# Performance work log

Hardware: AMD Instinct MI355X
Metric: run time of the kernel (lower is better)

The kernel has to match this reference:

```python
import jax, jax.numpy as jnp
import numpy as np
import math

EPS = 1e-15
R_CUT = 5.0
BERN_K = 16
FEAT = 128
N_ATOMS = 16384
N_EDGES = 100000
# log binomial(BERN_K-1, k) for the Bernstein radial basis
LOG_BINOM = np.array([math.lgamma(BERN_K) - math.lgamma(k + 1) - math.lgamma(BERN_K - k)
                      for k in range(BERN_K)], dtype=np.float32)


def swish(x, a, b):
    # learnable swish: a * x * sigmoid(b * x)
    return a * x * jax.nn.sigmoid(b * x)


def resmlp(x, W1, b1, W2, b2, Wout, aa, bb):
    # Residual( PreAct(lin1) -> PreAct(lin2) ) -> act -> Linear(no bias)
    h = swish(x, aa[0], bb[0]) @ W1.T + b1
    h = swish(h, aa[1], bb[1]) @ W2.T + b2
    y = x + h
    return swish(y, aa[2], bb[2]) @ Wout.T


def sph_harm(u, l):
    ux, uy, uz = u[:, 0], u[:, 1], u[:, 2]
    if l == 0:
        return jnp.ones((u.shape[0], 1), u.dtype)
    if l == 1:
        return jnp.stack([uy, uz, ux], axis=-1)
    s3 = 3.0 ** 0.5
    return jnp.stack([s3 * ux * uy, s3 * uy * uz, 0.5 * (3.0 * uz ** 2 - 1.0),
                      s3 * ux * uz, 0.5 * s3 * (ux ** 2 - uy ** 2)], axis=-1)


def bernstein_rho(r, gamma):
    # rho_k(r) = C(K-1,k) x^k (1-x)^(K-1-k) * f_cut(r), x = exp(-gamma r)
    k = jnp.arange(BERN_K, dtype=r.dtype)
    x = jnp.exp(-gamma * r)[:, None]                      # (E,1)
    bern = jnp.exp(jnp.asarray(LOG_BINOM)) * x ** k * (1.0 - x) ** (BERN_K - 1 - k)
    inside = r < R_CUT
    denom = jnp.where(inside, R_CUT ** 2 - r ** 2, 1.0)
    fcut = jnp.where(inside, jnp.exp(-r ** 2 / denom), 0.0)
    return bern * fcut[:, None]                           # (E,K)


def setup_inputs() -> dict:
    key = jax.random.key(0)
    ks = jax.random.split(key, 16)
    D, K = FEAT, BERN_K
    sc = 1.0 / (D ** 0.5)
    inp = {
        'xyz': jax.random.normal(ks[0], (N_ATOMS, 3), jnp.float32),
        'x_tilde': jax.random.normal(ks[1], (N_ATOMS, D), jnp.float32),
        'nbrs': jax.random.randint(ks[2], (N_EDGES, 2), 0, N_ATOMS),
        # 5 ResidualMLPs stacked: order [c, s, p, d, l]
        'W1': jax.random.normal(ks[3], (5, D, D), jnp.float32) * sc,
        'b1': jnp.zeros((5, D), jnp.float32),
        'W2': jax.random.normal(ks[4], (5, D, D), jnp.float32) * sc,
        'b2': jnp.zeros((5, D), jnp.float32),
        'Wout': jax.random.normal(ks[5], (5, D, D), jnp.float32) * sc,
        'act_a': jnp.ones((5, 3), jnp.float32),
        'act_b': jnp.full((5, 3), 1.702, jnp.float32),
        'G_s': jax.random.normal(ks[6], (D, K), jnp.float32) * (1.0 / K ** 0.5),
        'G_p': jax.random.normal(ks[7], (D, K), jnp.float32) * (1.0 / K ** 0.5),
        'G_d': jax.random.normal(ks[8], (D, K), jnp.float32) * (1.0 / K ** 0.5),
        'P_1': jax.random.normal(ks[9], (D, D), jnp.float32) * sc,
        'P_2': jax.random.normal(ks[10], (D, D), jnp.float32) * sc,
        'D_1': jax.random.normal(ks[11], (D, D), jnp.float32) * sc,
        'D_2': jax.random.normal(ks[12], (D, D), jnp.float32) * sc,
        'gamma': jnp.asarray(0.5, jnp.float32),
    }
    return inp


def reference(xyz, x_tilde, nbrs, W1, b1, W2, b2, Wout, act_a, act_b,
              G_s, G_p, G_d, P_1, P_2, D_1, D_2, gamma):
    N = xyz.shape[0]
    src = nbrs[:, 0]
    dst = nbrs[:, 1]
    r_ij = xyz[dst] - xyz[src]                            # (E,3)
    r = jnp.sqrt((r_ij ** 2 + EPS).sum(-1))               # stable norm, (E,)
    u = r_ij / r[:, None]
    rho = bernstein_rho(r, gamma)                         # (E,K)
    x_j = x_tilde[dst]                                    # (E,D)

    def mlp(x, i):
        return resmlp(x, W1[i], b1[i], W2[i], b2[i], Wout[i], act_a[i], act_b[i])

    c_term = mlp(x_tilde, 0)                              # (N,D)

    quants = []
    for i, (l, G) in enumerate([(0, G_s), (1, G_p), (2, G_d)]):
        y = sph_harm(u, l)                                # (E,M)
        # fused g_matmul: G @ (rho (x) y) -> (E,D,M), avoids (E,K,M) temp
        gm = jnp.einsum('dk,ek,em->edm', G, rho, y)
        feat = mlp(x_j, i + 1)                            # (E,D)
        per_nbr = feat[:, :, None] * gm                   # (E,D,M)
        quants.append(jax.ops.segment_sum(per_nbr, src, num_segments=N))

    def take_inner(q, M1, M2):
        t1 = jnp.einsum('ij,njm->nim', M1, q)
        t2 = jnp.einsum('ij,njm->nim', M2, q)
        return (t1 * t2).sum(-1)                          # (N,D)

    inp = c_term + quants[0][:, :, 0] \
        + take_inner(quants[1], P_1, P_2) + take_inner(quants[2], D_1, D_2)
    return mlp(inp, 4)
```

## Files before the change

kernel.cpp:

```cpp
#include <hip/hip_runtime.h>
#include <math.h>

#define D 128

typedef __attribute__((ext_vector_type(8))) short short8v;
typedef __attribute__((ext_vector_type(4))) float f32x4;
typedef __attribute__((ext_vector_type(4))) unsigned int uint4v;

__device__ __forceinline__ float fast_swish(float v, float a, float b) {
  float e = __builtin_amdgcn_exp2f(-1.4426950408889634f * (b * v));
  return a * v * __builtin_amdgcn_rcpf(1.0f + e);
}

__device__ __forceinline__ void bf16split_rne(float v, unsigned short& h, unsigned short& l) {
  unsigned int u = __float_as_uint(v);
  unsigned int rh = (u + 0x7FFFu + ((u >> 16) & 1u)) & 0xFFFF0000u;
  h = (unsigned short)(rh >> 16);
  float lf = v - __uint_as_float(rh);
  unsigned int u2 = __float_as_uint(lf);
  unsigned int rl = u2 + 0x7FFFu + ((u2 >> 16) & 1u);
  l = (unsigned short)(rl >> 16);
}

__device__ __forceinline__ void bf16split_fast(float v, unsigned short& h, unsigned short& l) {
  unsigned int u = __float_as_uint(v);
  h = (unsigned short)(u >> 16);
  float lf = v - __uint_as_float(u & 0xFFFF0000u);
  unsigned int u2 = __float_as_uint(lf);
  l = (unsigned short)((u2 + 0x7FFFu + ((u2 >> 16) & 1u)) >> 16);
}

template <bool SW>
__device__ __forceinline__ void stage16(const float* __restrict__ src, int lane,
                                        unsigned short* shHi, unsigned short* shLo,
                                        float a, float b) {
#pragma unroll
  for (int i = 0; i < 4; ++i) {
    int t = lane + 64 * i;
    int r = t >> 4, c = t & 15;
    const float4 v0 = *(const float4*)(src + r * D + c * 8);
    const float4 v1 = *(const float4*)(src + r * D + c * 8 + 4);
    float vv[8] = {v0.x, v0.y, v0.z, v0.w, v1.x, v1.y, v1.z, v1.w};
    unsigned int hw[4], lw[4];
#pragma unroll
    for (int jj = 0; jj < 4; ++jj) {
      float x0 = SW ? fast_swish(vv[2 * jj], a, b) : vv[2 * jj];
      float x1 = SW ? fast_swish(vv[2 * jj + 1], a, b) : vv[2 * jj + 1];
      unsigned short h0, l0, h1, l1;
      bf16split_fast(x0, h0, l0);
      bf16split_fast(x1, h1, l1);
      hw[jj] = (unsigned int)h0 | ((unsigned int)h1 << 16);
      lw[jj] = (unsigned int)l0 | ((unsigned int)l1 << 16);
    }
    int off = (c * 16) ^ ((r & 7) << 4);
    uint4v hv = {hw[0], hw[1], hw[2], hw[3]};
    uint4v lv = {lw[0], lw[1], lw[2], lw[3]};
    *(uint4v*)((char*)(shHi + r * D) + off) = hv;
    *(uint4v*)((char*)(shLo + r * D) + off) = lv;
  }
}

__device__ __forceinline__ void load_afrags(const unsigned short* sh, int lane, short8v* f) {
  int rl = lane & 15, q = lane >> 4;
  const char* base = (const char*)(sh + rl * D);
#pragma unroll
  for (int kc = 0; kc < 4; ++kc) {
    int off = (kc * 64 + q * 16) ^ ((rl & 7) << 4);
    f[kc] = *(const short8v*)(base + off);
  }
}

__device__ __forceinline__ void gemm16(const short8v* ah, const short8v* al,
                                       const unsigned short* __restrict__ prep, int m,
                                       int lane, f32x4* accs) {
  const short8v* ph = (const short8v*)(prep + (size_t)(2 * m) * 16384);
  const short8v* pl = (const short8v*)(prep + (size_t)(2 * m + 1) * 16384);
#pragma unroll
  for (int nt = 0; nt < 8; ++nt) {
    f32x4 acc = {0.f, 0.f, 0.f, 0.f};
#pragma unroll
    for (int kc = 0; kc < 4; ++kc) {
      int ci = (nt * 4 + kc) * 64 + lane;
      short8v bh = ph[ci];
      short8v bl = pl[ci];
      acc = __builtin_amdgcn_mfma_f32_16x16x32_bf16(al[kc], bh, acc, 0, 0, 0);
      acc = __builtin_amdgcn_mfma_f32_16x16x32_bf16(ah[kc], bl, acc, 0, 0, 0);
      acc = __builtin_amdgcn_mfma_f32_16x16x32_bf16(ah[kc], bh, acc, 0, 0, 0);
    }
    accs[nt] = acc;
  }
}

__global__ void prep_weights_kernel(const float* __restrict__ W1, const float* __restrict__ W2,
                                    const float* __restrict__ Wo, const float* __restrict__ P1,
                                    const float* __restrict__ P2, const float* __restrict__ D1,
                                    const float* __restrict__ D2, unsigned short* __restrict__ prep) {
  int t = blockIdx.x * 256 + threadIdx.x;
  if (t >= 19 * 2048) return;
  int m = t >> 11;
  int rem = t & 2047;
  int nt = rem >> 8;
  int kc = (rem >> 6) & 3;
  int lane = rem & 63;
  const float* src;
  if (m < 5) src = W1 + (size_t)m * 16384;
  else if (m < 10) src = W2 + (size_t)(m - 5) * 16384;
  else if (m < 15) src = Wo + (size_t)(m - 10) * 16384;
  else if (m == 15) src = P1;
  else if (m == 16) src = P2;
  else if (m == 17) src = D1;
  else src = D2;
  int row = nt * 16 + (lane & 15);
  int k0 = kc * 32 + (lane >> 4) * 8;
  unsigned int hw[4], lw[4];
#pragma unroll
  for (int jj = 0; jj < 4; ++jj) {
    unsigned short h0, l0, h1, l1;
    bf16split_rne(src[row * D + k0 + 2 * jj], h0, l0);
    bf16split_rne(src[row * D + k0 + 2 * jj + 1], h1, l1);
    hw[jj] = (unsigned int)h0 | ((unsigned int)h1 << 16);
    lw[jj] = (unsigned int)l0 | ((unsigned int)l1 << 16);
  }
  size_t chunk = (size_t)((nt * 4 + kc) * 64 + lane);
  uint4v hv = {hw[0], hw[1], hw[2], hw[3]};
  uint4v lv = {lw[0], lw[1], lw[2], lw[3]};
  *(uint4v*)(prep + (size_t)(2 * m) * 16384 + chunk * 8) = hv;
  *(uint4v*)(prep + (size_t)(2 * m + 1) * 16384 + chunk * 8) = lv;
}

__global__ __launch_bounds__(256) void resmlp_mfma(
    const float* __restrict__ xin, const unsigned short* __restrict__ prep,
    const float* __restrict__ b1b, const float* __restrict__ b2b,
    const float* __restrict__ act_a, const float* __restrict__ act_b,
    float* __restrict__ outbase, int branch_off, int n_atoms)
{
  __shared__ __align__(16) unsigned short shHiA[4][16 * D];
  __shared__ __align__(16) unsigned short shLoA[4][16 * D];
  const int lane = threadIdx.x & 63;
  const int wid = threadIdx.x >> 6;
  unsigned short* shHi = shHiA[wid];
  unsigned short* shLo = shLoA[wid];
  const int atom0 = (blockIdx.x * 4 + wid) * 16;
  const int br = blockIdx.y + branch_off;
  const float* b1 = b1b + br * D;
  const float* b2 = b2b + br * D;
  const float a0 = act_a[br * 3 + 0], g0 = act_b[br * 3 + 0];
  const float a1 = act_a[br * 3 + 1], g1 = act_b[br * 3 + 1];
  const float a2 = act_a[br * 3 + 2], g2 = act_b[br * 3 + 2];
  float* out = outbase + (size_t)blockIdx.y * n_atoms * D;
  const float* x0 = xin + (size_t)atom0 * D;

  stage16<true>(x0, lane, shHi, shLo, a0, g0);

  const int rl = lane & 15;
  const int rowq = (lane >> 4) * 4;
  short8v ah[4], al[4];
  f32x4 accs[8];

  load_afrags(shHi, lane, ah);
  load_afrags(shLo, lane, al);
  gemm16(ah, al, prep, br, lane, accs);
#pragma unroll
  for (int nt = 0; nt < 8; ++nt) {
    int col = nt * 16 + rl;
    float bv = b1[col];
#pragma unroll
    for (int r = 0; r < 4; ++r) {
      int row = rowq + r;
      float s = fast_swish(accs[nt][r] + bv, a1, g1);
      unsigned short h, l;
      bf16split_fast(s, h, l);
      int off = (col * 2) ^ ((row & 7) << 4);
      *(unsigned short*)((char*)(shHi + row * D) + off) = h;
      *(unsigned short*)((char*)(shLo + row * D) + off) = l;
    }
  }

  load_afrags(shHi, lane, ah);
  load_afrags(shLo, lane, al);
  gemm16(ah, al, prep, 5 + br, lane, accs);
#pragma unroll
  for (int nt = 0; nt < 8; ++nt) {
    int col = nt * 16 + rl;
    float bv = b2[col];
#pragma unroll
    for (int r = 0; r < 4; ++r) {
      int row = rowq + r;
      float y = x0[row * D + col] + accs[nt][r] + bv;
      float s = fast_swish(y, a2, g2);
      unsigned short h, l;
      bf16split_fast(s, h, l);
      int off = (col * 2) ^ ((row & 7) << 4);
      *(unsigned short*)((char*)(shHi + row * D) + off) = h;
      *(unsigned short*)((char*)(shLo + row * D) + off) = l;
    }
  }

  load_afrags(shHi, lane, ah);
  load_afrags(shLo, lane, al);
  gemm16(ah, al, prep, 10 + br, lane, accs);
#pragma unroll
  for (int nt = 0; nt < 8; ++nt)
#pragma unroll
    for (int r = 0; r < 4; ++r)
      out[(size_t)(atom0 + rowq + r) * D + nt * 16 + rl] = accs[nt][r];
}

__global__ __launch_bounds__(256) void inner_mfma(
    const float* __restrict__ q1, const float* __restrict__ q2,
    const unsigned short* __restrict__ prep,
    float* __restrict__ pA, float* __restrict__ pB, int n_atoms)
{
  __shared__ __align__(16) unsigned short shHiA[4][16 * D];
  __shared__ __align__(16) unsigned short shLoA[4][16 * D];
  const int lane = threadIdx.x & 63;
  const int wid = threadIdx.x >> 6;
  unsigned short* shHi = shHiA[wid];
  unsigned short* shLo = shLoA[wid];
  const int atom0 = (blockIdx.x * 4 + wid) * 16;
  const int g = blockIdx.y;
  const size_t nd = (size_t)n_atoms * D;
  const int rl = lane & 15;
  const int rowq = (lane >> 4) * 4;
  f32x4 eacc[8];
#pragma unroll
  for (int nt = 0; nt < 8; ++nt) eacc[nt] = f32x4{0.f, 0.f, 0.f, 0.f};

  for (int pp = 0; pp < 2; ++pp) {
    const int part = g * 2 + pp;
    const float* qp = (part < 3) ? q1 + (size_t)part * nd : q2 + (size_t)(part - 3) * nd;
    const int m1 = (part < 3) ? 15 : 17;
    stage16<false>(qp + (size_t)atom0 * D, lane, shHi, shLo, 0.f, 0.f);
    short8v ah[4], al[4];
    load_afrags(shHi, lane, ah);
    load_afrags(shLo, lane, al);
    const short8v* p1h = (const short8v*)(prep + (size_t)(2 * m1) * 16384);
    const short8v* p1l = (const short8v*)(prep + (size_t)(2 * m1 + 1) * 16384);
    const short8v* p2h = (const short8v*)(prep + (size_t)(2 * m1 + 2) * 16384);
    const short8v* p2l = (const short8v*)(prep + (size_t)(2 * m1 + 3) * 16384);
#pragma unroll
    for (int nt = 0; nt < 8; ++nt) {
      f32x4 t1 = {0.f, 0.f, 0.f, 0.f}, t2 = {0.f, 0.f, 0.f, 0.f};
#pragma unroll
      for (int kc = 0; kc < 4; ++kc) {
        int ci = (nt * 4 + kc) * 64 + lane;
        short8v b1h = p1h[ci], b1l = p1l[ci];
        short8v b2h = p2h[ci], b2l = p2l[ci];
        t1 = __builtin_amdgcn_mfma_f32_16x16x32_bf16(al[kc], b1h, t1, 0, 0, 0);
        t1 = __builtin_amdgcn_mfma_f32_16x16x32_bf16(ah[kc], b1l, t1, 0, 0, 0);
        t1 = __builtin_amdgcn_mfma_f32_16x16x32_bf16(ah[kc], b1h, t1, 0, 0, 0);
        t2 = __builtin_amdgcn_mfma_f32_16x16x32_bf16(al[kc], b2h, t2, 0, 0, 0);
        t2 = __builtin_amdgcn_mfma_f32_16x16x32_bf16(ah[kc], b2l, t2, 0, 0, 0);
        t2 = __builtin_amdgcn_mfma_f32_16x16x32_bf16(ah[kc], b2h, t2, 0, 0, 0);
      }
      eacc[nt] += t1 * t2;
    }
  }
  float* outp = (g < 3) ? (pA + (size_t)g * nd) : pB;
#pragma unroll
  for (int nt = 0; nt < 8; ++nt)
#pragma unroll
    for (int r = 0; r < 4; ++r)
      outp[(size_t)(atom0 + rowq + r) * D + nt * 16 + rl] = eacc[nt][r];
}

__global__ void edge_geom_kernel(const float* __restrict__ xyz,
                                 const int* __restrict__ nbrs,
                                 const float* __restrict__ gamma_p,
                                 float* __restrict__ rho_ws,
                                 float* __restrict__ y_ws, int n_edges)
{
  int e = blockIdx.x * 256 + threadIdx.x;
  if (e >= n_edges) return;
  int s = nbrs[2 * e], dd = nbrs[2 * e + 1];
  float rx = xyz[3 * dd + 0] - xyz[3 * s + 0];
  float ry = xyz[3 * dd + 1] - xyz[3 * s + 1];
  float rz = xyz[3 * dd + 2] - xyz[3 * s + 2];
  float r2 = rx * rx + ry * ry + rz * rz + 3e-15f;
  float r = sqrtf(r2);
  float inv = 1.0f / r;
  float ux = rx * inv, uy = ry * inv, uz = rz * inv;
  float gamma = gamma_p[0];
  float xv = __expf(-gamma * r);
  float omx = 1.0f - xv;
  float fcut = 0.0f;
  if (r < 5.0f) fcut = __expf(-r2 / (25.0f - r2));
  float xp[16], op[16];
  xp[0] = 1.f; op[0] = 1.f;
#pragma unroll
  for (int k = 1; k < 16; ++k) { xp[k] = xp[k - 1] * xv; op[k] = op[k - 1] * omx; }
  const float C[16] = {1.f, 15.f, 105.f, 455.f, 1365.f, 3003.f, 5005.f, 6435.f,
                       6435.f, 5005.f, 3003.f, 1365.f, 455.f, 105.f, 15.f, 1.f};
  float* rp = rho_ws + (size_t)e * 16;
#pragma unroll
  for (int k = 0; k < 16; ++k) rp[k] = C[k] * xp[k] * op[15 - k] * fcut;
  const float s3 = 1.7320508075688772f;
  float* yp = y_ws + (size_t)e * 8;
  yp[0] = uy; yp[1] = uz; yp[2] = ux;
  yp[3] = s3 * ux * uy; yp[4] = s3 * uy * uz; yp[5] = 0.5f * (3.f * uz * uz - 1.f);
  yp[6] = s3 * ux * uz; yp[7] = 0.5f * s3 * (ux * ux - uy * uy);
}

__global__ void hist_kernel(const int* __restrict__ nbrs, int* __restrict__ counts, int n_edges) {
  int e = blockIdx.x * 256 + threadIdx.x;
  if (e < n_edges) atomicAdd(&counts[nbrs[2 * e]], 1);
}

__global__ __launch_bounds__(1024) void scan_kernel(const int* __restrict__ counts,
                                                    int* __restrict__ offsets, int n) {
  __shared__ int part[1024];
  int tid = threadIdx.x;
  int base = tid * 16;
  int loc[16]; int s = 0;
#pragma unroll
  for (int i = 0; i < 16; ++i) {
    int c = (base + i < n) ? counts[base + i] : 0;
    loc[i] = c; s += c;
  }
  part[tid] = s;
  __syncthreads();
  for (int off = 1; off < 1024; off <<= 1) {
    int v = (tid >= off) ? part[tid - off] : 0;
    __syncthreads();
    part[tid] += v;
    __syncthreads();
  }
  int run = (tid == 0) ? 0 : part[tid - 1];
#pragma unroll
  for (int i = 0; i < 16; ++i) {
    if (base + i < n) offsets[base + i] = run;
    run += loc[i];
  }
}

__global__ void scatter_kernel(const int* __restrict__ nbrs, const int* __restrict__ offsets,
                               int* __restrict__ cursor, int* __restrict__ sorted, int n_edges) {
  int e = blockIdx.x * 256 + threadIdx.x;
  if (e < n_edges) {
    int s = nbrs[2 * e];
    int pos = offsets[s] + atomicAdd(&cursor[s], 1);
    sorted[pos] = e;
  }
}

__global__ __launch_bounds__(128) void aggregate_kernel(
    const float* __restrict__ rho_ws, const float* __restrict__ y_ws,
    const int* __restrict__ nbrs, const int* __restrict__ offsets,
    const int* __restrict__ counts, const int* __restrict__ sorted,
    const float* __restrict__ feat1, const float* __restrict__ feat2,
    const float* __restrict__ feat3,
    const float* __restrict__ Gs, const float* __restrict__ Gp,
    const float* __restrict__ Gd,
    float* __restrict__ q0, float* __restrict__ q1, float* __restrict__ q2,
    int n_atoms)
{
  int n = blockIdx.x;
  int d = threadIdx.x;
  float gs[16], gp[16], gd[16];
#pragma unroll
  for (int c = 0; c < 4; ++c) {
    float4 v = *(const float4*)&Gs[d * 16 + 4 * c];
    gs[4 * c] = v.x; gs[4 * c + 1] = v.y; gs[4 * c + 2] = v.z; gs[4 * c + 3] = v.w;
    v = *(const float4*)&Gp[d * 16 + 4 * c];
    gp[4 * c] = v.x; gp[4 * c + 1] = v.y; gp[4 * c + 2] = v.z; gp[4 * c + 3] = v.w;
    v = *(const float4*)&Gd[d * 16 + 4 * c];
    gd[4 * c] = v.x; gd[4 * c + 1] = v.y; gd[4 * c + 2] = v.z; gd[4 * c + 3] = v.w;
  }
  float a0 = 0.f, a1[3] = {0.f, 0.f, 0.f}, a2[5] = {0.f, 0.f, 0.f, 0.f, 0.f};
  int off = offsets[n], cnt = counts[n];
  for (int i = 0; i < cnt; ++i) {
    int e = sorted[off + i];
    int dst = nbrs[2 * e + 1];
    const float4* rp = (const float4*)(rho_ws + (size_t)e * 16);
    float4 r0v = rp[0], r1v = rp[1], r2v = rp[2], r3v = rp[3];
    float rho[16] = {r0v.x, r0v.y, r0v.z, r0v.w, r1v.x, r1v.y, r1v.z, r1v.w,
                     r2v.x, r2v.y, r2v.z, r2v.w, r3v.x, r3v.y, r3v.z, r3v.w};
    const float4* ypv = (const float4*)(y_ws + (size_t)e * 8);
    float4 y0v = ypv[0], y1v = ypv[1];
    float g_s = 0.f, g_p = 0.f, g_d = 0.f;
#pragma unroll
    for (int k = 0; k < 16; ++k) {
      g_s += gs[k] * rho[k];
      g_p += gp[k] * rho[k];
      g_d += gd[k] * rho[k];
    }
    float f1 = feat1[(size_t)dst * D + d];
    float f2 = feat2[(size_t)dst * D + d];
    float f3 = feat3[(size_t)dst * D + d];
    a0 += f1 * g_s;
    float ap = f2 * g_p;
    a1[0] += ap * y0v.x; a1[1] += ap * y0v.y; a1[2] += ap * y0v.z;
    float ad = f3 * g_d;
    a2[0] += ad * y0v.w; a2[1] += ad * y1v.x; a2[2] += ad * y1v.y;
    a2[3] += ad * y1v.z; a2[4] += ad * y1v.w;
  }
  q0[(size_t)n * D + d] = a0;
#pragma unroll
  for (int m = 0; m < 3; ++m) q1[((size_t)m * n_atoms + n) * D + d] = a1[m];
#pragma unroll
  for (int m = 0; m < 5; ++m) q2[((size_t)m * n_atoms + n) * D + d] = a2[m];
}

__global__ void assemble_kernel(const float* __restrict__ cterm,
                                const float* __restrict__ q0,
                                const float* __restrict__ pA,
                                const float* __restrict__ pB,
                                float* __restrict__ inp, int nd4)
{
  int i = blockIdx.x * 256 + threadIdx.x;
  if (i >= nd4) return;
  const float4* c = (const float4*)cterm;
  const float4* z = (const float4*)q0;
  const float4* a = (const float4*)pA;
  const float4* b = (const float4*)pB;
  float4 v = c[i], zz = z[i];
  float4 a0 = a[i], a1 = a[i + (size_t)nd4], a2 = a[i + 2 * (size_t)nd4], bb = b[i];
  float4 r;
  r.x = v.x + zz.x + a0.x + a1.x + a2.x + bb.x;
  r.y = v.y + zz.y + a0.y + a1.y + a2.y + bb.y;
  r.z = v.z + zz.z + a0.z + a1.z + a2.z + bb.z;
  r.w = v.w + zz.w + a0.w + a1.w + a2.w + bb.w;
  ((float4*)inp)[i] = r;
}

extern "C" void kernel_launch(void* const* d_in, const int* in_sizes, int n_in,
                              void* d_out, int out_size, void* d_ws, size_t ws_size,
                              hipStream_t stream)
{
  const float* xyz     = (const float*)d_in[0];
  const float* x_tilde = (const float*)d_in[1];
  const int*   nbrs    = (const int*)d_in[2];
  const float* W1      = (const float*)d_in[3];
  const float* b1      = (const float*)d_in[4];
  const float* W2      = (const float*)d_in[5];
  const float* b2      = (const float*)d_in[6];
  const float* Wout    = (const float*)d_in[7];
  const float* act_a   = (const float*)d_in[8];
  const float* act_b   = (const float*)d_in[9];
  const float* Gs      = (const float*)d_in[10];
  const float* Gp      = (const float*)d_in[11];
  const float* Gd      = (const float*)d_in[12];
  const float* P1      = (const float*)d_in[13];
  const float* P2      = (const float*)d_in[14];
  const float* D1m     = (const float*)d_in[15];
  const float* D2m     = (const float*)d_in[16];
  const float* gamma   = (const float*)d_in[17];
  float* out = (float*)d_out;

  const int n_atoms = in_sizes[0] / 3;
  const int n_edges = in_sizes[2] / 2;

  float* ws = (float*)d_ws;
  size_t nd = (size_t)n_atoms * D;
  float* feats  = ws;
  float* q0     = feats + 4 * nd;
  float* q1     = q0 + nd;
  float* q2     = q1 + 3 * nd;
  float* rho_ws = q2 + 5 * nd;
  float* y_ws   = rho_ws + (size_t)n_edges * 16;
  float* inp    = y_ws + (size_t)n_edges * 8;
  int* counts  = (int*)(inp + nd);
  int* offsets = counts + n_atoms;
  int* cursor  = offsets + n_atoms;
  int* sorted  = cursor + n_atoms;
  unsigned short* prep =
      (unsigned short*)(((uintptr_t)(sorted + n_edges) + 15) & ~(uintptr_t)15);

  float* pA = feats + nd;
  float* pB = rho_ws;

  hipMemsetAsync(counts, 0, (size_t)n_atoms * sizeof(int), stream);
  hipMemsetAsync(cursor, 0, (size_t)n_atoms * sizeof(int), stream);

  dim3 blk(256);
  int eb = (n_edges + 255) / 256;

  prep_weights_kernel<<<(19 * 2048 + 255) / 256, blk, 0, stream>>>(
      W1, W2, Wout, P1, P2, D1m, D2m, prep);

  resmlp_mfma<<<dim3(n_atoms / 64, 4), dim3(256), 0, stream>>>(
      x_tilde, prep, b1, b2, act_a, act_b, feats, 0, n_atoms);

  edge_geom_kernel<<<eb, blk, 0, stream>>>(xyz, nbrs, gamma, rho_ws, y_ws, n_edges);
  hist_kernel<<<eb, blk, 0, stream>>>(nbrs, counts, n_edges);
  scan_kernel<<<1, 1024, 0, stream>>>(counts, offsets, n_atoms);
  scatter_kernel<<<eb, blk, 0, stream>>>(nbrs, offsets, cursor, sorted, n_edges);

  aggregate_kernel<<<n_atoms, 128, 0, stream>>>(
      rho_ws, y_ws, nbrs, offsets, counts, sorted,
      feats + nd, feats + 2 * nd, feats + 3 * nd, Gs, Gp, Gd,
      q0, q1, q2, n_atoms);

  inner_mfma<<<dim3(n_atoms / 64, 4), dim3(256), 0, stream>>>(
      q1, q2, prep, pA, pB, n_atoms);

  assemble_kernel<<<(int)((nd / 4 + 255) / 256), blk, 0, stream>>>(
      feats, q0, pA, pB, inp, (int)(nd / 4));

  resmlp_mfma<<<dim3(n_atoms / 64, 1), dim3(256), 0, stream>>>(
      inp, prep, b1, b2, act_a, act_b, out, 4, n_atoms);
}
```

Measured before the change: 340.3 us.

## Share 64-row activation tile across warps, split output columns per warp

The resmlp and inner MFMA kernels now stage a shared 64-row activation tile per block instead of a private 16-row tile per warp. Each warp computes two 16-column output tiles across all 64 rows rather than all 128 columns for 16 rows. Each warp therefore loads only a quarter of the weight fragments from global or L2 and reuses each across four row tiles. The cost is block-wide __syncthreads between layers, and A fragments are now re-read from LDS for every k-chunk instead of being held in registers.

```diff
diff --git a/kernel.cpp b/kernel.cpp
--- a/kernel.cpp
+++ b/kernel.cpp
@@ -28,6 +28,13 @@
   float lf = v - __uint_as_float(u & 0xFFFF0000u);
   unsigned int u2 = __float_as_uint(lf);
   l = (unsigned short)((u2 + 0x7FFFu + ((u2 >> 16) & 1u)) >> 16);
+}
+
+__device__ __forceinline__ f32x4 mfma3(short8v ah, short8v al, short8v bh, short8v bl, f32x4 acc) {
+  acc = __builtin_amdgcn_mfma_f32_16x16x32_bf16(al, bh, acc, 0, 0, 0);
+  acc = __builtin_amdgcn_mfma_f32_16x16x32_bf16(ah, bl, acc, 0, 0, 0);
+  acc = __builtin_amdgcn_mfma_f32_16x16x32_bf16(ah, bh, acc, 0, 0, 0);
+  return acc;
 }
 
 template <bool SW>
@@ -57,37 +64,6 @@
     uint4v lv = {lw[0], lw[1], lw[2], lw[3]};
     *(uint4v*)((char*)(shHi + r * D) + off) = hv;
     *(uint4v*)((char*)(shLo + r * D) + off) = lv;
-  }
-}
-
-__device__ __forceinline__ void load_afrags(const unsigned short* sh, int lane, short8v* f) {
-  int rl = lane & 15, q = lane >> 4;
-  const char* base = (const char*)(sh + rl * D);
-#pragma unroll
-  for (int kc = 0; kc < 4; ++kc) {
-    int off = (kc * 64 + q * 16) ^ ((rl & 7) << 4);
-    f[kc] = *(const short8v*)(base + off);
-  }
-}
-
-__device__ __forceinline__ void gemm16(const short8v* ah, const short8v* al,
-                                       const unsigned short* __restrict__ prep, int m,
-                                       int lane, f32x4* accs) {
-  const short8v* ph = (const short8v*)(prep + (size_t)(2 * m) * 16384);
-  const short8v* pl = (const short8v*)(prep + (size_t)(2 * m + 1) * 16384);
-#pragma unroll
-  for (int nt = 0; nt < 8; ++nt) {
-    f32x4 acc = {0.f, 0.f, 0.f, 0.f};
-#pragma unroll
-    for (int kc = 0; kc < 4; ++kc) {
-      int ci = (nt * 4 + kc) * 64 + lane;
-      short8v bh = ph[ci];
-      short8v bl = pl[ci];
-      acc = __builtin_amdgcn_mfma_f32_16x16x32_bf16(al[kc], bh, acc, 0, 0, 0);
-      acc = __builtin_amdgcn_mfma_f32_16x16x32_bf16(ah[kc], bl, acc, 0, 0, 0);
-      acc = __builtin_amdgcn_mfma_f32_16x16x32_bf16(ah[kc], bh, acc, 0, 0, 0);
-    }
-    accs[nt] = acc;
   }
 }
 
@@ -134,13 +110,11 @@
     const float* __restrict__ act_a, const float* __restrict__ act_b,
     float* __restrict__ outbase, int branch_off, int n_atoms)
 {
-  __shared__ __align__(16) unsigned short shHiA[4][16 * D];
-  __shared__ __align__(16) unsigned short shLoA[4][16 * D];
+  __shared__ __align__(16) unsigned short shHi[64 * D];
+  __shared__ __align__(16) unsigned short shLo[64 * D];
   const int lane = threadIdx.x & 63;
   const int wid = threadIdx.x >> 6;
-  unsigned short* shHi = shHiA[wid];
-  unsigned short* shLo = shLoA[wid];
-  const int atom0 = (blockIdx.x * 4 + wid) * 16;
+  const int atom0 = blockIdx.x * 64;
   const int br = blockIdx.y + branch_off;
   const float* b1 = b1b + br * D;
   const float* b2 = b2b + br * D;
@@ -150,60 +124,92 @@
   float* out = outbase + (size_t)blockIdx.y * n_atoms * D;
   const float* x0 = xin + (size_t)atom0 * D;
 
-  stage16<true>(x0, lane, shHi, shLo, a0, g0);
+  stage16<true>(x0 + wid * 16 * D, lane, shHi + wid * 16 * D, shLo + wid * 16 * D, a0, g0);
+  __syncthreads();
 
   const int rl = lane & 15;
-  const int rowq = (lane >> 4) * 4;
-  short8v ah[4], al[4];
-  f32x4 accs[8];
-
-  load_afrags(shHi, lane, ah);
-  load_afrags(shLo, lane, al);
-  gemm16(ah, al, prep, br, lane, accs);
-#pragma unroll
-  for (int nt = 0; nt < 8; ++nt) {
-    int col = nt * 16 + rl;
+  const int q = lane >> 4;
+  const int rowq = q * 4;
+  const int nt0 = wid * 2;
+
+  f32x4 acc[4][2];
+
+#define GEMM_LAYER(mat)                                                        \
+  do {                                                                         \
+    const unsigned short* ph = prep + (size_t)(2 * (mat)) * 16384;             \
+    const unsigned short* pl = prep + (size_t)(2 * (mat) + 1) * 16384;         \
+    _Pragma("unroll") for (int mt = 0; mt < 4; ++mt)                           \
+        _Pragma("unroll") for (int j = 0; j < 2; ++j)                          \
+            acc[mt][j] = f32x4{0.f, 0.f, 0.f, 0.f};                            \
+    _Pragma("unroll") for (int kc = 0; kc < 4; ++kc) {                         \
+      int ci0 = (nt0 * 4 + kc) * 64 + lane;                                    \
+      int ci1 = ((nt0 + 1) * 4 + kc) * 64 + lane;                              \
+      short8v bh0 = *(const short8v*)(ph + (size_t)ci0 * 8);                   \
+      short8v bl0 = *(const short8v*)(pl + (size_t)ci0 * 8);                   \
+      short8v bh1 = *(const short8v*)(ph + (size_t)ci1 * 8);                   \
+      short8v bl1 = *(const short8v*)(pl + (size_t)ci1 * 8);                   \
+      int aoff = (kc * 64 + q * 16) ^ ((rl & 7) << 4);                         \
+      _Pragma("unroll") for (int mt = 0; mt < 4; ++mt) {                       \
+        short8v ah = *(const short8v*)((const char*)(shHi + (mt * 16 + rl) * D) + aoff); \
+        short8v al = *(const short8v*)((const char*)(shLo + (mt * 16 + rl) * D) + aoff); \
+        acc[mt][0] = mfma3(ah, al, bh0, bl0, acc[mt][0]);                      \
+        acc[mt][1] = mfma3(ah, al, bh1, bl1, acc[mt][1]);                      \
+      }                                                                        \
+    }                                                                          \
+  } while (0)
+
+  GEMM_LAYER(br);
+  __syncthreads();
+#pragma unroll
+  for (int j = 0; j < 2; ++j) {
+    int col = (nt0 + j) * 16 + rl;
     float bv = b1[col];
 #pragma unroll
-    for (int r = 0; r < 4; ++r) {
-      int row = rowq + r;
-      float s = fast_swish(accs[nt][r] + bv, a1, g1);
-      unsigned short h, l;
-      bf16split_fast(s, h, l);
-      int off = (col * 2) ^ ((row & 7) << 4);
-      *(unsigned short*)((char*)(shHi + row * D) + off) = h;
-      *(unsigned short*)((char*)(shLo + row * D) + off) = l;
-    }
-  }
-
-  load_afrags(shHi, lane, ah);
-  load_afrags(shLo, lane, al);
-  gemm16(ah, al, prep, 5 + br, lane, accs);
-#pragma unroll
-  for (int nt = 0; nt < 8; ++nt) {
-    int col = nt * 16 + rl;
+    for (int mt = 0; mt < 4; ++mt)
+#pragma unroll
+      for (int r = 0; r < 4; ++r) {
+        int row = mt * 16 + rowq + r;
+        float s = fast_swish(acc[mt][j][r] + bv, a1, g1);
+        unsigned short h, l;
+        bf16split_fast(s, h, l);
+        int off = (col * 2) ^ ((row & 7) << 4);
+        *(unsigned short*)((char*)(shHi + row * D) + off) = h;
+        *(unsigned short*)((char*)(shLo + row * D) + off) = l;
+      }
+  }
+  __syncthreads();
+
+  GEMM_LAYER(5 + br);
+  __syncthreads();
+#pragma unroll
+  for (int j = 0; j < 2; ++j) {
+    int col = (nt0 + j) * 16 + rl;
     float bv = b2[col];
 #pragma unroll
-    for (int r = 0; r < 4; ++r) {
-      int row = rowq + r;
-      float y = x0[row * D + col] + accs[nt][r] + bv;
-      float s = fast_swish(y, a2, g2);
-      unsigned short h, l;
-      bf16split_fast(s, h, l);
-      int off = (col * 2) ^ ((row & 7) << 4);
-      *(unsigned short*)((char*)(shHi + row * D) + off) = h;
-      *(unsigned short*)((char*)(shLo + row * D) + off) = l;
-    }
-  }
-
-  load_afrags(shHi, lane, ah);
-  load_afrags(shLo, lane, al);
-  gemm16(ah, al, prep, 10 + br, lane, accs);
-#pragma unroll
-  for (int nt = 0; nt < 8; ++nt)
-#pragma unroll
-    for (int r = 0; r < 4; ++r)
-      out[(size_t)(atom0 + rowq + r) * D + nt * 16 + rl] = accs[nt][r];
+    for (int mt = 0; mt < 4; ++mt)
+#pragma unroll
+      for (int r = 0; r < 4; ++r) {
+        int row = mt * 16 + rowq + r;
+        float y = x0[row * D + col] + acc[mt][j][r] + bv;
+        float s = fast_swish(y, a2, g2);
+        unsigned short h, l;
+        bf16split_fast(s, h, l);
+        int off = (col * 2) ^ ((row & 7) << 4);
+        *(unsigned short*)((char*)(shHi + row * D) + off) = h;
+        *(unsigned short*)((char*)(shLo + row * D) + off) = l;
+      }
+  }
+  __syncthreads();
+
+  GEMM_LAYER(10 + br);
+#pragma unroll
+  for (int j = 0; j < 2; ++j)
+#pragma unroll
+    for (int mt = 0; mt < 4; ++mt)
+#pragma unroll
+      for (int r = 0; r < 4; ++r)
+        out[(size_t)(atom0 + mt * 16 + rowq + r) * D + (nt0 + j) * 16 + rl] = acc[mt][j][r];
+#undef GEMM_LAYER
 }
 
 __global__ __launch_bounds__(256) void inner_mfma(
@@ -211,57 +217,73 @@
     const unsigned short* __restrict__ prep,
     float* __restrict__ pA, float* __restrict__ pB, int n_atoms)
 {
-  __shared__ __align__(16) unsigned short shHiA[4][16 * D];
-  __shared__ __align__(16) unsigned short shLoA[4][16 * D];
+  __shared__ __align__(16) unsigned short shHi[64 * D];
+  __shared__ __align__(16) unsigned short shLo[64 * D];
   const int lane = threadIdx.x & 63;
   const int wid = threadIdx.x >> 6;
-  unsigned short* shHi = shHiA[wid];
-  unsigned short* shLo = shLoA[wid];
-  const int atom0 = (blockIdx.x * 4 + wid) * 16;
+  const int atom0 = blockIdx.x * 64;
   const int g = blockIdx.y;
   const size_t nd = (size_t)n_atoms * D;
   const int rl = lane & 15;
-  const int rowq = (lane >> 4) * 4;
-  f32x4 eacc[8];
-#pragma unroll
-  for (int nt = 0; nt < 8; ++nt) eacc[nt] = f32x4{0.f, 0.f, 0.f, 0.f};
+  const int q = lane >> 4;
+  const int rowq = q * 4;
+  const int nt0 = wid * 2;
+
+  f32x4 eacc[4][2];
+#pragma unroll
+  for (int mt = 0; mt < 4; ++mt)
+#pragma unroll
+    for (int j = 0; j < 2; ++j) eacc[mt][j] = f32x4{0.f, 0.f, 0.f, 0.f};
 
   for (int pp = 0; pp < 2; ++pp) {
     const int part = g * 2 + pp;
     const float* qp = (part < 3) ? q1 + (size_t)part * nd : q2 + (size_t)(part - 3) * nd;
     const int m1 = (part < 3) ? 15 : 17;
-    stage16<false>(qp + (size_t)atom0 * D, lane, shHi, shLo, 0.f, 0.f);
-    short8v ah[4], al[4];
-    load_afrags(shHi, lane, ah);
-    load_afrags(shLo, lane, al);
-    const short8v* p1h = (const short8v*)(prep + (size_t)(2 * m1) * 16384);
-    const short8v* p1l = (const short8v*)(prep + (size_t)(2 * m1 + 1) * 16384);
-    const short8v* p2h = (const short8v*)(prep + (size_t)(2 * m1 + 2) * 16384);
-    const short8v* p2l = (const short8v*)(prep + (size_t)(2 * m1 + 3) * 16384);
-#pragma unroll
-    for (int nt = 0; nt < 8; ++nt) {
-      f32x4 t1 = {0.f, 0.f, 0.f, 0.f}, t2 = {0.f, 0.f, 0.f, 0.f};
+    if (pp) __syncthreads();
+    stage16<false>(qp + (size_t)atom0 * D + wid * 16 * D, lane,
+                   shHi + wid * 16 * D, shLo + wid * 16 * D, 0.f, 0.f);
+    __syncthreads();
+    const unsigned short* p1h = prep + (size_t)(2 * m1) * 16384;
+    const unsigned short* p1l = prep + (size_t)(2 * m1 + 1) * 16384;
+    const unsigned short* p2h = prep + (size_t)(2 * m1 + 2) * 16384;
+    const unsigned short* p2l = prep + (size_t)(2 * m1 + 3) * 16384;
+#pragma unroll
+    for (int j = 0; j < 2; ++j) {
+      f32x4 t1[4], t2[4];
+#pragma unroll
+      for (int mt = 0; mt < 4; ++mt) {
+        t1[mt] = f32x4{0.f, 0.f, 0.f, 0.f};
+        t2[mt] = f32x4{0.f, 0.f, 0.f, 0.f};
+      }
 #pragma unroll
       for (int kc = 0; kc < 4; ++kc) {
-        int ci = (nt * 4 + kc) * 64 + lane;
-        short8v b1h = p1h[ci], b1l = p1l[ci];
-        short8v b2h = p2h[ci], b2l = p2l[ci];
-        t1 = __builtin_amdgcn_mfma_f32_16x16x32_bf16(al[kc], b1h, t1, 0, 0, 0);
-        t1 = __builtin_amdgcn_mfma_f32_16x16x32_bf16(ah[kc], b1l, t1, 0, 0, 0);
-        t1 = __builtin_amdgcn_mfma_f32_16x16x32_bf16(ah[kc], b1h, t1, 0, 0, 0);
-        t2 = __builtin_amdgcn_mfma_f32_16x16x32_bf16(al[kc], b2h, t2, 0, 0, 0);
-        t2 = __builtin_amdgcn_mfma_f32_16x16x32_bf16(ah[kc], b2l, t2, 0, 0, 0);
-        t2 = __builtin_amdgcn_mfma_f32_16x16x32_bf16(ah[kc], b2h, t2, 0, 0, 0);
+        int ci = ((nt0 + j) * 4 + kc) * 64 + lane;
+        short8v b1h = *(const short8v*)(p1h + (size_t)ci * 8);
+        short8v b1l = *(const short8v*)(p1l + (size_t)ci * 8);
+        short8v b2h = *(const short8v*)(p2h + (size_t)ci * 8);
+        short8v b2l = *(const short8v*)(p2l + (size_t)ci * 8);
+        int aoff = (kc * 64 + q * 16) ^ ((rl & 7) << 4);
+#pragma unroll
+        for (int mt = 0; mt < 4; ++mt) {
+          short8v ah = *(const short8v*)((const char*)(shHi + (mt * 16 + rl) * D) + aoff);
+          short8v al = *(const short8v*)((const char*)(shLo + (mt * 16 + rl) * D) + aoff);
+          t1[mt] = mfma3(ah, al, b1h, b1l, t1[mt]);
+          t2[mt] = mfma3(ah, al, b2h, b2l, t2[mt]);
+        }
       }
-      eacc[nt] += t1 * t2;
+#pragma unroll
+      for (int mt = 0; mt < 4; ++mt) eacc[mt][j] += t1[mt] * t2[mt];
     }
   }
+
   float* outp = (g < 3) ? (pA + (size_t)g * nd) : pB;
 #pragma unroll
-  for (int nt = 0; nt < 8; ++nt)
-#pragma unroll
-    for (int r = 0; r < 4; ++r)
-      outp[(size_t)(atom0 + rowq + r) * D + nt * 16 + rl] = eacc[nt][r];
+  for (int j = 0; j < 2; ++j)
+#pragma unroll
+    for (int mt = 0; mt < 4; ++mt)
+#pragma unroll
+      for (int r = 0; r < 4; ++r)
+        outp[(size_t)(atom0 + mt * 16 + rowq + r) * D + (nt0 + j) * 16 + rl] = eacc[mt][j][r];
 }
 
 __global__ void edge_geom_kernel(const float* __restrict__ xyz,
```

New measurement: 274.6 us. -19.3%, faster.
